# Performance work log

Hardware: AMD Instinct MI355X
Metric: run time of the kernel (lower is better)

## Reference

```python
import jax, jax.numpy as jnp
import numpy as np

N = 50000
F_IN = 512
H1 = 500
H2 = 100
C = 16
E = 800000


def setup_inputs() -> dict:
    key = jax.random.key(0)
    ks = jax.random.split(key, 8)
    x = jax.random.normal(ks[0], (N, F_IN), dtype=jnp.float32)
    edge_index = jax.random.randint(ks[1], (2, E), 0, N, dtype=jnp.int64)
    W1 = jax.random.normal(ks[2], (F_IN, H1), dtype=jnp.float32) / np.sqrt(F_IN)
    b1 = jnp.zeros((H1,), dtype=jnp.float32)
    W2 = jax.random.normal(ks[3], (H1, H2), dtype=jnp.float32) / np.sqrt(H1)
    b2 = jnp.zeros((H2,), dtype=jnp.float32)
    W3 = jax.random.normal(ks[4], (H2, C), dtype=jnp.float32) / np.sqrt(H2)
    b3 = jnp.zeros((C,), dtype=jnp.float32)
    return {"x": x, "edge_index": edge_index, "W1": W1, "b1": b1,
            "W2": W2, "b2": b2, "W3": W3, "b3": b3}


def _edge_norm(edge_index, num_nodes):
    # add self loops (as in torch add_self_loops), then symmetric degree norm
    loops = jnp.arange(num_nodes, dtype=edge_index.dtype)
    row = jnp.concatenate([edge_index[0], loops])
    col = jnp.concatenate([edge_index[1], loops])
    deg = jax.ops.segment_sum(jnp.ones_like(row, dtype=jnp.float32), row,
                              num_segments=num_nodes)
    dinv = jnp.where(deg > 0, deg ** -0.5, 0.0)  # norm[isinf] = 0
    norm = dinv[row] * dinv[col]
    return row, col, norm


def _graph_conv(x, row, col, norm, W, b, num_nodes):
    h = x @ W + b                                  # [N, out]
    msg = norm[:, None] * h[col]                   # gather + scale, [E', out]
    return jax.ops.segment_sum(msg, row, num_segments=num_nodes)  # SpMM


def reference(x, edge_index, W1, b1, W2, b2, W3, b3):
    num_nodes = x.shape[0]
    row, col, norm = _edge_norm(edge_index, num_nodes)
    h = jnp.tanh(_graph_conv(x, row, col, norm, W1, b1, num_nodes))
    h = jnp.tanh(_graph_conv(h, row, col, norm, W2, b2, num_nodes))
    h = jnp.tanh(_graph_conv(h, row, col, norm, W3, b3, num_nodes))
    return jax.nn.softmax(h, axis=1)
```

## Files before the change

### kernel.cpp

```cpp
#include <hip/hip_runtime.h>
#include <math.h>

#define NN  50000
#define FIN 512
#define HH1 500
#define HH2 100
#define NC  16
#define NE  800000
#define KD  512
#define LDP 40

typedef __attribute__((ext_vector_type(4))) float    f32x4;
typedef __attribute__((ext_vector_type(4))) _Float16 f16x4;
typedef __attribute__((ext_vector_type(8))) _Float16 f16x8;
typedef __attribute__((ext_vector_type(8))) unsigned short u16x8;


__global__ void zero2_k(int* a, int* b) {
    int i = blockIdx.x * blockDim.x + threadIdx.x;
    if (i < NN) { a[i] = 0; b[i] = 0; }
}

__global__ void hist_k(const int* __restrict__ rows, int* __restrict__ rowcnt) {
    int i = blockIdx.x * blockDim.x + threadIdx.x;
    if (i < NE) atomicAdd(&rowcnt[rows[i]], 1);
}

__global__ void dinv_k(const int* __restrict__ rowcnt, float* __restrict__ dinv) {
    int i = blockIdx.x * blockDim.x + threadIdx.x;
    if (i < NN) dinv[i] = rsqrtf((float)(rowcnt[i] + 1));
}

__global__ __launch_bounds__(1024) void scan1_k(const int* __restrict__ cnt,
                                                int* __restrict__ excl,
                                                int* __restrict__ bsum) {
    __shared__ int s[1024];
    int t = threadIdx.x;
    int i = blockIdx.x * 1024 + t;
    int v = (i < NN) ? cnt[i] : 0;
    s[t] = v;
    __syncthreads();
    #pragma unroll
    for (int off = 1; off < 1024; off <<= 1) {
        int add = (t >= off) ? s[t - off] : 0;
        __syncthreads();
        s[t] += add;
        __syncthreads();
    }
    if (i < NN) excl[i] = s[t] - v;
    if (t == 1023) bsum[blockIdx.x] = s[1023];
}

__global__ void scan2_k(int* bsum, int nb) {
    int lane = threadIdx.x;
    int orig = (lane < nb) ? bsum[lane] : 0;
    int v = orig;
    #pragma unroll
    for (int off = 1; off < 64; off <<= 1) {
        int u = __shfl_up(v, off, 64);
        if (lane >= off) v += u;
    }
    if (lane < nb) bsum[lane] = v - orig;
}

__global__ void scan3_k(const int* __restrict__ excl, const int* __restrict__ bsum,
                        int* __restrict__ ptr) {
    int i = blockIdx.x * 256 + threadIdx.x;
    if (i < NN) ptr[i] = excl[i] + bsum[i >> 10];
}

__global__ void scatter_k(const int* __restrict__ rows, const int* __restrict__ cols,
                          const float* __restrict__ dinv,
                          const int* __restrict__ row_ptr, int* __restrict__ fill,
                          int2* __restrict__ cw) {
    int e = blockIdx.x * blockDim.x + threadIdx.x;
    if (e >= NE) return;
    int r = rows[e], c = cols[e];
    int pos = row_ptr[r] + atomicAdd(&fill[r], 1);
    cw[pos] = make_int2(c, __float_as_int(dinv[r] * dinv[c]));
}


#define R1 (512 * 512)
#define R2 (128 * 512)
#define R3 (128 * 128)

__global__ void wconv3_k(const float* __restrict__ W1, const float* __restrict__ W2,
                         const float* __restrict__ W3, _Float16* __restrict__ Wt1,
                         _Float16* __restrict__ Wt2, _Float16* __restrict__ Wt3)
{
    int idx = blockIdx.x * 256 + threadIdx.x;
    if (idx < R1) {
        int n_ = idx >> 9, kk = idx & 511;
        float v = (n_ < HH1) ? W1[(size_t)kk * HH1 + n_] : 0.0f;
        Wt1[idx] = (_Float16)v;
    } else if (idx < R1 + R2) {
        int j = idx - R1;
        int n_ = j >> 9, kk = j & 511;
        float v = (kk < HH1 && n_ < HH2) ? W2[(size_t)kk * HH2 + n_] : 0.0f;
        Wt2[j] = (_Float16)v;
    } else if (idx < R1 + R2 + R3) {
        int j = idx - R1 - R2;
        int n_ = j >> 7, kk = j & 127;
        float v = (kk < HH2 && n_ < NC) ? W3[(size_t)kk * NC + n_] : 0.0f;
        Wt3[j] = (_Float16)v;
    }
}


template<int AF16, int KDIM>
__global__ __launch_bounds__(256) void gemm_f16_k(
    const void* __restrict__ Av, const _Float16* __restrict__ Wt,
    const float* __restrict__ bias, _Float16* __restrict__ Cb,
    int mpad, int n, int m)
{
    __shared__ __align__(16) _Float16 As[128 * LDP];
    __shared__ __align__(16) _Float16 Bs[128 * LDP];

    const float*    Af32 = (const float*)Av;
    const _Float16* Af16 = (const _Float16*)Av;

    int tid  = threadIdx.x;
    int lane = tid & 63;
    int wid  = tid >> 6;
    int wrow = wid & 1, wcol = wid >> 1;
    int lr = lane & 15, q = lane >> 4;
    int row0 = blockIdx.x * 128, col0 = blockIdx.y * 128;

    f32x4 acc[4][4];
    #pragma unroll
    for (int i = 0; i < 4; i++)
        #pragma unroll
        for (int j = 0; j < 4; j++) acc[i][j] = (f32x4){0.f, 0.f, 0.f, 0.f};

    float4 pa32[4];
    u16x8  pa16[2];
    u16x8  pb[2];

    auto load_pf = [&](int kt) {
        if (AF16 == 0) {
            #pragma unroll
            for (int i = 0; i < 4; i++) {
                int idx = tid + i * 256;
                int rr = idx >> 3, c4 = idx & 7;
                int gr = row0 + rr;
                pa32[i] = (gr < n) ? *(const float4*)(Af32 + (size_t)gr * KDIM + kt + c4 * 4)
                                   : make_float4(0.f, 0.f, 0.f, 0.f);
            }
        } else {
            #pragma unroll
            for (int i = 0; i < 2; i++) {
                int idx = tid + i * 256;
                int rr = idx >> 2, c8 = idx & 3;
                int gr = row0 + rr;
                pa16[i] = (gr < n) ? *(const u16x8*)(Af16 + (size_t)gr * KDIM + kt + c8 * 8)
                                   : (u16x8){0, 0, 0, 0, 0, 0, 0, 0};
            }
        }
        #pragma unroll
        for (int i = 0; i < 2; i++) {
            int idx = tid + i * 256;
            int rr = idx >> 2, c8 = idx & 3;
            pb[i] = *(const u16x8*)(Wt + (size_t)(col0 + rr) * KDIM + kt + c8 * 8);
        }
    };

    load_pf(0);

    for (int step = 0; step < KDIM / 32; step++) {
        __syncthreads();
        if (AF16 == 0) {
            #pragma unroll
            for (int i = 0; i < 4; i++) {
                int idx = tid + i * 256;
                int rr = idx >> 3, c4 = idx & 7;
                float4 v = pa32[i];
                f16x4 hv = {(_Float16)v.x, (_Float16)v.y, (_Float16)v.z, (_Float16)v.w};
                *(f16x4*)(As + rr * LDP + c4 * 4) = hv;
            }
        } else {
            #pragma unroll
            for (int i = 0; i < 2; i++) {
                int idx = tid + i * 256;
                int rr = idx >> 2, c8 = idx & 3;
                *(u16x8*)(As + rr * LDP + c8 * 8) = pa16[i];
            }
        }
        #pragma unroll
        for (int i = 0; i < 2; i++) {
            int idx = tid + i * 256;
            int rr = idx >> 2, c8 = idx & 3;
            *(u16x8*)(Bs + rr * LDP + c8 * 8) = pb[i];
        }
        __syncthreads();

        if (step + 1 < KDIM / 32) load_pf((step + 1) * 32);

        f16x8 a[4], b[4];
        #pragma unroll
        for (int t = 0; t < 4; t++) {
            a[t] = *(const f16x8*)(As + (wrow * 64 + t * 16 + lr) * LDP + q * 8);
            b[t] = *(const f16x8*)(Bs + (wcol * 64 + t * 16 + lr) * LDP + q * 8);
        }
        #pragma unroll
        for (int ti = 0; ti < 4; ti++)
            #pragma unroll
            for (int tj = 0; tj < 4; tj++)
                acc[ti][tj] = __builtin_amdgcn_mfma_f32_16x16x32_f16(
                    a[ti], b[tj], acc[ti][tj], 0, 0, 0);
    }

    #pragma unroll
    for (int ti = 0; ti < 4; ti++) {
        #pragma unroll
        for (int tj = 0; tj < 4; tj++) {
            int col = col0 + wcol * 64 + tj * 16 + lr;
            if (col >= mpad) continue;
            bool valid = col < m;
            float bv = valid ? bias[col] : 0.0f;
            #pragma unroll
            for (int p = 0; p < 4; p++) {
                int row = row0 + wrow * 64 + ti * 16 + q * 4 + p;
                if (row < n) {
                    float v = valid ? (acc[ti][tj][p] + bv) : 0.0f;
                    Cb[(size_t)row * mpad + col] = (_Float16)v;
                }
            }
        }
    }
}


__device__ __forceinline__ void fma_mix8(float* acc, u16x8 v, float w) {
    union { u16x8 u; unsigned int d[4]; } t; t.u = v;
    #pragma unroll
    for (int k = 0; k < 4; k++) {
        asm("v_fma_mix_f32 %0, %1, %2, %0 op_sel:[0,0,0] op_sel_hi:[1,0,0]"
            : "+v"(acc[2 * k]) : "v"(t.d[k]), "v"(w));
        asm("v_fma_mix_f32 %0, %1, %2, %0 op_sel:[1,0,0] op_sel_hi:[1,0,0]"
            : "+v"(acc[2 * k + 1]) : "v"(t.d[k]), "v"(w));
    }
}


__global__ __launch_bounds__(256) void spmm_f16_500_k(
    const int* __restrict__ row_ptr, const int* __restrict__ rowcnt,
    const int2* __restrict__ cw, const float* __restrict__ dinv,
    const _Float16* __restrict__ hb, _Float16* __restrict__ outh)
{
    int r = blockIdx.x * 4 + (threadIdx.x >> 6);
    int lane = threadIdx.x & 63;
    if (r >= NN) return;

    const u16x8* h8 = (const u16x8*)hb;

    float acc[8];
    #pragma unroll
    for (int i = 0; i < 8; i++) acc[i] = 0.f;

    float d = dinv[r];
    fma_mix8(acc, h8[(size_t)r * 64 + lane], d * d);

    int beg = row_ptr[r], cnt = rowcnt[r];
    for (int base = 0; base < cnt; base += 64) {
        int m = (cnt - base < 64) ? (cnt - base) : 64;
        int2 vc = (lane < m) ? cw[beg + base + lane] : make_int2(0, 0);
        int P = (m + 7) & ~7;
        for (int j = 0; j < P; j += 8) {
            u16x8 vv[8]; float wl[8];
            #pragma unroll
            for (int u = 0; u < 8; u++) {
                int c  = __builtin_amdgcn_readlane(vc.x, j + u);
                int wb = __builtin_amdgcn_readlane(vc.y, j + u);
                wl[u] = __int_as_float(wb);
                vv[u] = h8[(size_t)c * 64 + lane];
            }
            #pragma unroll
            for (int u = 0; u < 8; u++) fma_mix8(acc, vv[u], wl[u]);
        }
    }

    int f0 = lane * 8;
    f16x8 o;
    #pragma unroll
    for (int i = 0; i < 8; i++)
        o[i] = (_Float16)((f0 + i < HH1) ? tanhf(acc[i]) : 0.0f);
    __builtin_nontemporal_store(o, (f16x8*)(outh + (size_t)r * KD + f0));
}


__global__ __launch_bounds__(256) void spmm_f16_100_k(
    const int* __restrict__ row_ptr, const int* __restrict__ rowcnt,
    const int2* __restrict__ cw, const float* __restrict__ dinv,
    const _Float16* __restrict__ hb, _Float16* __restrict__ outh)
{
    int r = blockIdx.x * 16 + (threadIdx.x >> 4);
    int lane = threadIdx.x & 15;
    if (r >= NN) return;

    const u16x8* h8 = (const u16x8*)hb;

    float acc[8];
    #pragma unroll
    for (int i = 0; i < 8; i++) acc[i] = 0.f;

    float d = dinv[r];
    fma_mix8(acc, h8[(size_t)r * 16 + lane], d * d);

    int beg = row_ptr[r], cnt = rowcnt[r];
    int j = 0;
    for (; j + 7 < cnt; j += 8) {
        int2  e[8];
        u16x8 v[8];
        #pragma unroll
        for (int u = 0; u < 8; u++) e[u] = cw[beg + j + u];
        #pragma unroll
        for (int u = 0; u < 8; u++) v[u] = h8[(size_t)e[u].x * 16 + lane];
        #pragma unroll
        for (int u = 0; u < 8; u++) fma_mix8(acc, v[u], __int_as_float(e[u].y));
    }
    for (; j < cnt; j++) {
        int2 e = cw[beg + j];
        fma_mix8(acc, h8[(size_t)e.x * 16 + lane], __int_as_float(e.y));
    }

    int f0 = lane * 8;
    f16x8 o;
    #pragma unroll
    for (int i = 0; i < 8; i++)
        o[i] = (_Float16)((f0 + i < HH2) ? tanhf(acc[i]) : 0.0f);
    __builtin_nontemporal_store(o, (f16x8*)(outh + (size_t)r * 128 + f0));
}


__global__ __launch_bounds__(256) void spmm3h_k(
    const int* __restrict__ row_ptr, const int* __restrict__ rowcnt,
    const int2* __restrict__ cw, const float* __restrict__ dinv,
    const _Float16* __restrict__ hb, float* __restrict__ out)
{
    int r = blockIdx.x * 128 + (threadIdx.x >> 1);
    int lane = threadIdx.x & 1;
    if (r >= NN) return;

    const u16x8* h8 = (const u16x8*)hb;

    float acc[8];
    #pragma unroll
    for (int i = 0; i < 8; i++) acc[i] = 0.f;

    float d = dinv[r];
    fma_mix8(acc, h8[(size_t)r * 2 + lane], d * d);

    int beg = row_ptr[r], cnt = rowcnt[r];
    int j = 0;
    for (; j + 3 < cnt; j += 4) {
        int2  e0 = cw[beg + j],     e1 = cw[beg + j + 1];
        int2  e2 = cw[beg + j + 2], e3 = cw[beg + j + 3];
        u16x8 v0 = h8[(size_t)e0.x * 2 + lane];
        u16x8 v1 = h8[(size_t)e1.x * 2 + lane];
        u16x8 v2 = h8[(size_t)e2.x * 2 + lane];
        u16x8 v3 = h8[(size_t)e3.x * 2 + lane];
        fma_mix8(acc, v0, __int_as_float(e0.y));
        fma_mix8(acc, v1, __int_as_float(e1.y));
        fma_mix8(acc, v2, __int_as_float(e2.y));
        fma_mix8(acc, v3, __int_as_float(e3.y));
    }
    for (; j < cnt; j++) {
        int2 e = cw[beg + j];
        fma_mix8(acc, h8[(size_t)e.x * 2 + lane], __int_as_float(e.y));
    }

    float* o = out + (size_t)r * NC + lane * 8;
    f32x4 a0 = {acc[0], acc[1], acc[2], acc[3]};
    f32x4 a1 = {acc[4], acc[5], acc[6], acc[7]};
    __builtin_nontemporal_store(a0, (f32x4*)o);
    __builtin_nontemporal_store(a1, (f32x4*)(o + 4));
}

__global__ void tanh_softmax_k(const float* __restrict__ in, float* __restrict__ out) {
    int r = blockIdx.x * blockDim.x + threadIdx.x;
    if (r >= NN) return;
    float v[NC];
    float mx = -1e30f;
    #pragma unroll
    for (int j = 0; j < NC; j++) {
        v[j] = tanhf(in[r * NC + j]);
        mx = fmaxf(mx, v[j]);
    }
    float s = 0.0f;
    #pragma unroll
    for (int j = 0; j < NC; j++) { v[j] = expf(v[j] - mx); s += v[j]; }
    float inv = 1.0f / s;
    #pragma unroll
    for (int j = 0; j < NC; j++) out[r * NC + j] = v[j] * inv;
}


extern "C" void kernel_launch(void* const* d_in, const int* in_sizes, int n_in,
                              void* d_out, int out_size, void* d_ws, size_t ws_size,
                              hipStream_t stream)
{
    const float* x  = (const float*)d_in[0];
    const int*   ei = (const int*)d_in[1];
    const float* W1 = (const float*)d_in[2];
    const float* b1 = (const float*)d_in[3];
    const float* W2 = (const float*)d_in[4];
    const float* b2 = (const float*)d_in[5];
    const float* W3 = (const float*)d_in[6];
    const float* b3 = (const float*)d_in[7];
    float* out = (float*)d_out;

    const int* rows = ei;
    const int* cols = ei + NE;

    char* p = (char*)d_ws;
    float*     dinv    = (float*)p;     p += (size_t)NN * 4;
    int*       rowcnt  = (int*)p;       p += (size_t)NN * 4;
    int*       row_ptr = (int*)p;       p += (size_t)NN * 4;
    int*       fill    = (int*)p;       p += (size_t)NN * 4;
    int*       excl    = (int*)p;       p += (size_t)NN * 4;
    int*       bsum    = (int*)p;       p += (size_t)256 * 4;
    int2*      cw      = (int2*)p;      p += (size_t)NE * 8;
    float*     B3      = (float*)p;     p += (size_t)NN * NC * 4;
    _Float16*  A1h     = (_Float16*)p;  p += (size_t)NN * KD * 2;
    _Float16*  h1h     = (_Float16*)p;  p += (size_t)NN * KD * 2;
    _Float16*  A2h     = (_Float16*)p;  p += (size_t)NN * 128 * 2;
    _Float16*  h2h     = (_Float16*)p;  p += (size_t)NN * 128 * 2;
    _Float16*  A3h     = (_Float16*)p;  p += (size_t)NN * NC * 2;
    _Float16*  Wt1     = (_Float16*)p;  p += (size_t)R1 * 2;
    _Float16*  Wt2     = (_Float16*)p;  p += (size_t)R2 * 2;
    _Float16*  Wt3     = (_Float16*)p;  p += (size_t)R3 * 2;

    const int T = 256;
    const int NB = (NN + 1023) / 1024;

    wconv3_k<<<(R1 + R2 + R3) / 256, T, 0, stream>>>(W1, W2, W3, Wt1, Wt2, Wt3);
    zero2_k<<<(NN + T - 1) / T, T, 0, stream>>>(rowcnt, fill);
    hist_k<<<(NE + T - 1) / T, T, 0, stream>>>(rows, rowcnt);
    dinv_k<<<(NN + T - 1) / T, T, 0, stream>>>(rowcnt, dinv);
    scan1_k<<<NB, 1024, 0, stream>>>(rowcnt, excl, bsum);
    scan2_k<<<1, 64, 0, stream>>>(bsum, NB);
    scan3_k<<<(NN + T - 1) / T, T, 0, stream>>>(excl, bsum, row_ptr);
    scatter_k<<<(NE + T - 1) / T, T, 0, stream>>>(rows, cols, dinv, row_ptr, fill, cw);

    {
        dim3 g((NN + 127) / 128, 4);
        gemm_f16_k<0, 512><<<g, T, 0, stream>>>(x, Wt1, b1, A1h, KD, NN, HH1);
        spmm_f16_500_k<<<(NN + 3) / 4, T, 0, stream>>>(row_ptr, rowcnt, cw,
                                                       dinv, A1h, h1h);
    }
    {
        dim3 g((NN + 127) / 128, 1);
        gemm_f16_k<1, 512><<<g, T, 0, stream>>>(h1h, Wt2, b2, A2h, 128, NN, HH2);
        spmm_f16_100_k<<<(NN + 15) / 16, T, 0, stream>>>(row_ptr, rowcnt, cw,
                                                         dinv, A2h, h2h);
    }
    {
        dim3 g((NN + 127) / 128, 1);
        gemm_f16_k<1, 128><<<g, T, 0, stream>>>(h2h, Wt3, b3, A3h, NC, NN, NC);
        spmm3h_k<<<(NN + 127) / 128, T, 0, stream>>>(row_ptr, rowcnt, cw,
                                                     dinv, A3h, B3);
        tanh_softmax_k<<<(NN + T - 1) / T, T, 0, stream>>>(B3, out);
    }
}
```

Baseline: 550.1 us.

## Split layer-1 aggregation into two column-half passes for cache locality

Result: no change. 551.0 us (+0.2%).

```diff
diff --git a/kernel.cpp b/kernel.cpp
--- a/kernel.cpp
+++ b/kernel.cpp
@@ -14,6 +14,7 @@
 typedef __attribute__((ext_vector_type(4))) _Float16 f16x4;
 typedef __attribute__((ext_vector_type(8))) _Float16 f16x8;
 typedef __attribute__((ext_vector_type(8))) unsigned short u16x8;
+typedef __attribute__((ext_vector_type(4))) unsigned short u16x4;
 
 
 __global__ void zero2_k(int* a, int* b) {
@@ -108,7 +109,7 @@
 }
 
 
-template<int AF16, int KDIM>
+template<int AF16, int KDIM, int COUT>
 __global__ __launch_bounds__(256) void gemm_f16_k(
     const void* __restrict__ Av, const _Float16* __restrict__ Wt,
     const float* __restrict__ bias, _Float16* __restrict__ Cb,
@@ -223,7 +224,13 @@
                 int row = row0 + wrow * 64 + ti * 16 + q * 4 + p;
                 if (row < n) {
                     float v = valid ? (acc[ti][tj][p] + bv) : 0.0f;
-                    Cb[(size_t)row * mpad + col] = (_Float16)v;
+                    if (COUT == 1) {
+                        size_t addr = (size_t)(col >> 8) * ((size_t)NN * 256)
+                                    + (size_t)row * 256 + (col & 255);
+                        Cb[addr] = (_Float16)v;
+                    } else {
+                        Cb[(size_t)row * mpad + col] = (_Float16)v;
+                    }
                 }
             }
         }
@@ -242,24 +249,36 @@
     }
 }
 
-
-__global__ __launch_bounds__(256) void spmm_f16_500_k(
+__device__ __forceinline__ void fma_mix4(float* acc, u16x4 v, float w) {
+    union { u16x4 u; unsigned int d[2]; } t; t.u = v;
+    #pragma unroll
+    for (int k = 0; k < 2; k++) {
+        asm("v_fma_mix_f32 %0, %1, %2, %0 op_sel:[0,0,0] op_sel_hi:[1,0,0]"
+            : "+v"(acc[2 * k]) : "v"(t.d[k]), "v"(w));
+        asm("v_fma_mix_f32 %0, %1, %2, %0 op_sel:[1,0,0] op_sel_hi:[1,0,0]"
+            : "+v"(acc[2 * k + 1]) : "v"(t.d[k]), "v"(w));
+    }
+}
+
+
+__global__ __launch_bounds__(256) void spmm_f16_256_k(
     const int* __restrict__ row_ptr, const int* __restrict__ rowcnt,
     const int2* __restrict__ cw, const float* __restrict__ dinv,
-    const _Float16* __restrict__ hb, _Float16* __restrict__ outh)
+    const _Float16* __restrict__ hc,
+    _Float16* __restrict__ outh, int fbase)
 {
     int r = blockIdx.x * 4 + (threadIdx.x >> 6);
     int lane = threadIdx.x & 63;
     if (r >= NN) return;
 
-    const u16x8* h8 = (const u16x8*)hb;
-
-    float acc[8];
-    #pragma unroll
-    for (int i = 0; i < 8; i++) acc[i] = 0.f;
+    const u16x4* h4 = (const u16x4*)hc;
+
+    float acc[4];
+    #pragma unroll
+    for (int i = 0; i < 4; i++) acc[i] = 0.f;
 
     float d = dinv[r];
-    fma_mix8(acc, h8[(size_t)r * 64 + lane], d * d);
+    fma_mix4(acc, h4[(size_t)r * 64 + lane], d * d);
 
     int beg = row_ptr[r], cnt = rowcnt[r];
     for (int base = 0; base < cnt; base += 64) {
@@ -267,25 +286,25 @@
         int2 vc = (lane < m) ? cw[beg + base + lane] : make_int2(0, 0);
         int P = (m + 7) & ~7;
         for (int j = 0; j < P; j += 8) {
-            u16x8 vv[8]; float wl[8];
+            u16x4 vv[8]; float wl[8];
             #pragma unroll
             for (int u = 0; u < 8; u++) {
                 int c  = __builtin_amdgcn_readlane(vc.x, j + u);
                 int wb = __builtin_amdgcn_readlane(vc.y, j + u);
                 wl[u] = __int_as_float(wb);
-                vv[u] = h8[(size_t)c * 64 + lane];
-            }
-            #pragma unroll
-            for (int u = 0; u < 8; u++) fma_mix8(acc, vv[u], wl[u]);
-        }
-    }
-
-    int f0 = lane * 8;
-    f16x8 o;
-    #pragma unroll
-    for (int i = 0; i < 8; i++)
+                vv[u] = h4[(size_t)c * 64 + lane];
+            }
+            #pragma unroll
+            for (int u = 0; u < 8; u++) fma_mix4(acc, vv[u], wl[u]);
+        }
+    }
+
+    int f0 = fbase + lane * 4;
+    f16x4 o;
+    #pragma unroll
+    for (int i = 0; i < 4; i++)
         o[i] = (_Float16)((f0 + i < HH1) ? tanhf(acc[i]) : 0.0f);
-    __builtin_nontemporal_store(o, (f16x8*)(outh + (size_t)r * KD + f0));
+    __builtin_nontemporal_store(o, (f16x4*)(outh + (size_t)r * KD + f0));
 }
 
 
@@ -445,19 +464,21 @@
 
     {
         dim3 g((NN + 127) / 128, 4);
-        gemm_f16_k<0, 512><<<g, T, 0, stream>>>(x, Wt1, b1, A1h, KD, NN, HH1);
-        spmm_f16_500_k<<<(NN + 3) / 4, T, 0, stream>>>(row_ptr, rowcnt, cw,
-                                                       dinv, A1h, h1h);
+        gemm_f16_k<0, 512, 1><<<g, T, 0, stream>>>(x, Wt1, b1, A1h, KD, NN, HH1);
+        spmm_f16_256_k<<<(NN + 3) / 4, T, 0, stream>>>(row_ptr, rowcnt, cw, dinv,
+                                                       A1h, h1h, 0);
+        spmm_f16_256_k<<<(NN + 3) / 4, T, 0, stream>>>(row_ptr, rowcnt, cw, dinv,
+                                                       A1h + (size_t)NN * 256, h1h, 256);
     }
     {
         dim3 g((NN + 127) / 128, 1);
-        gemm_f16_k<1, 512><<<g, T, 0, stream>>>(h1h, Wt2, b2, A2h, 128, NN, HH2);
+        gemm_f16_k<1, 512, 0><<<g, T, 0, stream>>>(h1h, Wt2, b2, A2h, 128, NN, HH2);
         spmm_f16_100_k<<<(NN + 15) / 16, T, 0, stream>>>(row_ptr, rowcnt, cw,
                                                          dinv, A2h, h2h);
     }
     {
         dim3 g((NN + 127) / 128, 1);
-        gemm_f16_k<1, 128><<<g, T, 0, stream>>>(h2h, Wt3, b3, A3h, NC, NN, NC);
+        gemm_f16_k<1, 128, 0><<<g, T, 0, stream>>>(h2h, Wt3, b3, A3h, NC, NN, NC);
         spmm3h_k<<<(NN + 127) / 128, T, 0, stream>>>(row_ptr, rowcnt, cw,
                                                      dinv, A3h, B3);
         tanh_softmax_k<<<(NN + T - 1) / T, T, 0, stream>>>(B3, out);
```
